# Performance work log

Hardware: AMD Instinct MI355X
Metric: run time of the kernel (lower is better)

Reference implementation:

```python
import jax, jax.numpy as jnp
import numpy as np

P = 8      # patch_size
DIM = 16   # per-head channel dim
HEADS = 4
LN_EPS = 1e-6


def _conv_patch(x, W, b):
    # stride=kernel=P patch conv; SAME degenerates to VALID when H%P==0
    y = jax.lax.conv_general_dilated(
        x, W, window_strides=(P, P), padding='VALID',
        dimension_numbers=('NHWC', 'HWIO', 'NHWC'))
    return y + b


def _proj_heads(x, W, b):
    # b h w (c p0 p1 head) -> b head (h p0) (w p1) c
    y = _conv_patch(x, W, b)
    B, hh, ww, _ = y.shape
    y = y.reshape(B, hh, ww, DIM, P, P, HEADS)
    y = y.transpose(0, 6, 1, 4, 2, 5, 3)            # b head hh p0 ww p1 c
    return y.reshape(B, HEADS, hh * P, ww * P, DIM)


def _to_patch(t):
    # n head (h p1) (w p2) c -> n head c h w p1 p2
    B, hd, H, W, c = t.shape
    t = t.reshape(B, hd, H // P, P, W // P, P, c)
    return t.transpose(0, 1, 6, 2, 4, 3, 5)


def _from_patch(t):
    # n head c h w p1 p2 -> n head (h p1) (w p2) c
    B, hd, c, hh, ww, _, _ = t.shape
    t = t.transpose(0, 1, 3, 5, 4, 6, 2)
    return t.reshape(B, hd, hh * P, ww * P, c)


def setup_inputs() -> dict:
    key = jax.random.key(0)
    ks = jax.random.split(key, 6)
    B, H, W, Cin = 4, 256, 256, 16
    feat = DIM * HEADS * P * P  # 4096
    s_qkv = 0.02
    inp = {
        'x': jax.random.normal(ks[0], (B, H, W, Cin), jnp.float32),
        'Wq': jax.random.normal(ks[1], (P, P, Cin, feat), jnp.float32) * s_qkv,
        'bq': jnp.zeros((feat,), jnp.float32),
        'Wk': jax.random.normal(ks[2], (P, P, Cin, feat), jnp.float32) * s_qkv,
        'bk': jnp.zeros((feat,), jnp.float32),
        'Wv': jax.random.normal(ks[3], (P, P, Cin, feat), jnp.float32) * s_qkv,
        'bv': jnp.zeros((feat,), jnp.float32),
        'ln_scale': jnp.ones((DIM,), jnp.float32),
        'ln_bias': jnp.zeros((DIM,), jnp.float32),
        'Wout': jax.random.normal(ks[4], (P, P, HEADS * DIM, DIM * P * P), jnp.float32) * 0.02,
        'bout': jnp.zeros((DIM * P * P,), jnp.float32),
    }
    return inp


def reference(x, Wq, bq, Wk, bk, Wv, bv, ln_scale, ln_bias, Wout, bout):
    q = _proj_heads(x, Wq, bq)  # [B, heads, H, W, dim]
    k = _proj_heads(x, Wk, bk)
    v = _proj_heads(x, Wv, bv)

    # frequency-domain 'attention': per-8x8-patch rfft2 multiply irfft2
    qf = jnp.fft.rfft2(_to_patch(q))
    kf = jnp.fft.rfft2(_to_patch(k))
    out = jnp.fft.irfft2(qf * kf, s=(P, P))
    out = _from_patch(out)                          # [B, heads, H, W, dim]

    # LayerNorm over channel dim (flax default eps=1e-6, scale+bias)
    mu = out.mean(-1, keepdims=True)
    var = ((out - mu) ** 2).mean(-1, keepdims=True)
    out = (out - mu) * jax.lax.rsqrt(var + LN_EPS) * ln_scale + ln_bias

    out = v * out
    # b head h w c -> b h w (head c)
    B, hd, H, W, c = out.shape
    out = out.transpose(0, 2, 3, 1, 4).reshape(B, H, W, hd * c)

    # output projection (no heads): conv then b h w (c p0 p1) -> b (h p0) (w p1) c
    y = _conv_patch(out, Wout, bout)
    Bo, hh, ww, _ = y.shape
    y = y.reshape(Bo, hh, ww, DIM, P, P).transpose(0, 1, 4, 2, 5, 3)
    return y.reshape(Bo, hh * P, ww * P, DIM)
```

## Files before the change

kernel.cpp:

```cpp
#include <hip/hip_runtime.h>
#include <hip/hip_bf16.h>
#include <cstdint>
#include <cstddef>

typedef float  f32x4  __attribute__((ext_vector_type(4)));
typedef __bf16 bf16x8 __attribute__((ext_vector_type(8)));
typedef __bf16 bf16x4 __attribute__((ext_vector_type(4)));


#define GLOAD_LDS16(gp, lp)                                                     \
    __builtin_amdgcn_global_load_lds(                                           \
        (const __attribute__((address_space(1))) void*)(gp),                    \
        (__attribute__((address_space(3))) void*)(lp), 16, 0, 0)

#define MFMA16(d, a, b) d = __builtin_amdgcn_mfma_f32_16x16x32_bf16(a, b, d, 0, 0, 0)

#define BAR() asm volatile("s_barrier" ::: "memory")

__global__ __launch_bounds__(256) void k_im2col(const float* __restrict__ x,
                                                __bf16* __restrict__ Xb)
{
    const int p = blockIdx.x;
    const int t = threadIdx.x;
    const int b = p >> 10, hh = (p >> 5) & 31, ww = p & 31;
    const int e = t * 4;
    const int c = e & 15, ij = e >> 4;
    const int i = ij >> 3, j = ij & 7;
    const size_t src = ((((size_t)(b * 256 + hh * 8 + i)) * 256) + (ww * 8 + j)) * 16 + c;
    f32x4 v = *(const f32x4*)(x + src);
    bf16x4 o;
    o[0] = (__bf16)v[0]; o[1] = (__bf16)v[1]; o[2] = (__bf16)v[2]; o[3] = (__bf16)v[3];
    *(bf16x4*)(Xb + (size_t)p * 1024 + e) = o;
}

__global__ __launch_bounds__(256) void k_wqkvT(const float* __restrict__ Wq,
                                               const float* __restrict__ Wk,
                                               const float* __restrict__ Wv,
                                               __bf16* __restrict__ WT)
{
    __shared__ float tile[64][261];
    int q = blockIdx.x;
    const int t = threadIdx.x;
    const int kb = q & 15;   q >>= 4;
    const int ch = q & 15;   q >>= 4;
    const int s  = q;
    const int k0 = kb * 64;
    const float* __restrict__ W = (s == 0) ? Wq : (s == 1) ? Wk : Wv;

#pragma unroll
    for (int rep = 0; rep < 16; rep++) {
        const int idx = rep * 256 + t;
        const int kl = idx >> 6, col4 = (idx & 63) * 4;
        const f32x4 v = *(const f32x4*)(W + (size_t)(k0 + kl) * 4096 + ch * 256 + col4);
        tile[kl][col4 + 0] = v[0];
        tile[kl][col4 + 1] = v[1];
        tile[kl][col4 + 2] = v[2];
        tile[kl][col4 + 3] = v[3];
    }
    __syncthreads();
    const size_t nbase = (size_t)s * 4096 + ch * 64;
#pragma unroll
    for (int rep = 0; rep < 64; rep++) {
        const int idx = rep * 256 + t;
        const int kl = idx & 63;
        const int rest = idx >> 6;
        const int p = rest & 63, h = rest >> 6;
        WT[(nbase + h * 1024 + p) * 1024 + k0 + kl] = (__bf16)tile[kl][p * 4 + h];
    }
}

__global__ __launch_bounds__(256) void k_biasperm(const float* __restrict__ bq,
                                                  const float* __restrict__ bk,
                                                  const float* __restrict__ bv,
                                                  float* __restrict__ bp)
{
    const int n = blockIdx.x * 256 + threadIdx.x;
    const int s = n >> 12;
    const int r = n & 4095;
    const int head = r >> 10, c = (r >> 6) & 15, pp = r & 63;
    const float* __restrict__ b = (s == 0) ? bq : (s == 1) ? bk : bv;
    bp[n] = b[c * 256 + pp * 4 + head];
}

__global__ __launch_bounds__(256) void k_woutT(const float* __restrict__ Wo,
                                               __bf16* __restrict__ WT)
{
    __shared__ float tile[64][129];
    const int q = blockIdx.x;
    const int t = threadIdx.x;
    const int n0 = (q & 15) * 64;
    const int k0 = (q >> 4) * 128;
    const int ch = n0 >> 6;
#pragma unroll
    for (int rep = 0; rep < 32; rep++) {
        const int idx = rep * 256 + t;
        const int kl = idx >> 6, nn = idx & 63;
        tile[nn][kl] = Wo[(size_t)(k0 + kl) * 1024 + n0 + nn];
    }
    __syncthreads();
#pragma unroll
    for (int rep = 0; rep < 32; rep++) {
        const int idx = rep * 256 + t;
        const int nn = idx >> 7, kl = idx & 127;
        const int no = ((nn >> 3) & 7) * 128 + (nn & 7) * 16 + ch;
        WT[(size_t)no * 4096 + k0 + kl] = (__bf16)tile[nn][kl];
    }
}

__device__ __forceinline__ void stage_half(const __bf16* __restrict__ mat,
                                           const int gRow0, const int K,
                                           const int k0, __bf16* lds, const int t)
{
    const int w6 = (t >> 6) << 6;
#pragma unroll
    for (int r = 0; r < 2; r++) {
        const int idx = r * 512 + t;
        const int row = idx >> 3;
        const int colb = ((t & 7) << 4) ^ ((row & 7) << 4);
        const char* gp = (const char*)(mat + (size_t)(gRow0 + row) * K + k0) + colb;
        GLOAD_LDS16(gp, (char*)lds + (size_t)(r * 512 + w6) * 16);
    }
}

__global__ __launch_bounds__(512, 1) void gemm256(const __bf16* __restrict__ A,
                                                  const __bf16* __restrict__ Bt,
                                                  __bf16* __restrict__ C,
                                                  const float* __restrict__ bias,
                                                  const int M, const int N,
                                                  const int K, const int nby)
{
    __shared__ __bf16 As[2][256 * 64];
    __shared__ __bf16 Bs[2][256 * 64];

    const int t = threadIdx.x;
    const int l = t & 63, w = t >> 6;
    const int wr = w >> 2, wc = w & 3;

    const int nwg = (int)gridDim.x, cpx = nwg >> 3;
    const int bid = (int)blockIdx.x;
    const int sbid = (bid & 7) * cpx + (bid >> 3);
    const int bm = sbid % nby, bn = sbid / nby;
    const int row0 = bm * 256, col0 = bn * 256;

    const int lrow = l & 15;
    const int lkb  = (l >> 4) << 4;
    const int lswz = (l & 7) << 4;
    const int ce0 = ((0  + lkb) ^ lswz) >> 1;
    const int ce1 = ((64 + lkb) ^ lswz) >> 1;

    const int arow = wr * 128 + lrow;
    const int brow = wc * 64 + lrow;

    const int NT = K >> 6;
    f32x4 acc[8][4] = {};
    bf16x8 a0[4][2], a1[4][2], b[4][2];

    stage_half(A,  row0,       K, 0,  As[0],        t);
    stage_half(A,  row0 + 128, K, 0,  As[0] + 8192, t);
    stage_half(A,  row0,       K, 64, As[1],        t);
    stage_half(A,  row0 + 128, K, 64, As[1] + 8192, t);
    stage_half(Bt, col0,       K, 0,  Bs[0],        t);
    stage_half(Bt, col0 + 128, K, 0,  Bs[0] + 8192, t);
    asm volatile("s_waitcnt vmcnt(0)" ::: "memory");
    BAR();
#pragma unroll
    for (int mi = 0; mi < 4; ++mi) {
        const int rr = (arow + mi * 16) * 64;
        a0[mi][0] = *(const bf16x8*)&As[0][rr + ce0];
        a0[mi][1] = *(const bf16x8*)&As[0][rr + ce1];
    }

    int cur = 0;
    for (int it = 0; it < NT; ++it) {
        const __bf16* AsC = As[cur];
        const __bf16* AsN = As[cur ^ 1];
        const __bf16* BsC = Bs[cur];
        __bf16* BsN = Bs[cur ^ 1];
        const bool stB = (it + 1 < NT);
        const bool stA = (it + 2 < NT);
        const bool pfA = (it + 1 < NT);
        const int kB = (it + 1) << 6;
        const int kA = (it + 2) << 6;

        BAR();
#pragma unroll
        for (int ni = 0; ni < 4; ++ni) {
            const int rr = (brow + ni * 16) * 64;
            b[ni][0] = *(const bf16x8*)&BsC[rr + ce0];
            b[ni][1] = *(const bf16x8*)&BsC[rr + ce1];
        }
#pragma unroll
        for (int mi = 0; mi < 4; ++mi) {
            const int rr = (arow + 64 + mi * 16) * 64;
            a1[mi][0] = *(const bf16x8*)&AsC[rr + ce0];
            a1[mi][1] = *(const bf16x8*)&AsC[rr + ce1];
        }
        if (stB) {
            stage_half(Bt, col0,       K, kB, BsN,        t);
            stage_half(Bt, col0 + 128, K, kB, BsN + 8192, t);
        }
        __builtin_amdgcn_s_setprio(1);
#pragma unroll
        for (int mi = 0; mi < 4; ++mi)
#pragma unroll
            for (int ni = 0; ni < 4; ++ni) {
                MFMA16(acc[mi][ni], a0[mi][0], b[ni][0]);
                MFMA16(acc[mi][ni], a0[mi][1], b[ni][1]);
            }
        __builtin_amdgcn_s_setprio(0);
        if (pfA)
            asm volatile("s_waitcnt vmcnt(4)" ::: "memory");

        BAR();
        if (pfA) {
#pragma unroll
            for (int mi = 0; mi < 4; ++mi) {
                const int rr = (arow + mi * 16) * 64;
                a0[mi][0] = *(const bf16x8*)&AsN[rr + ce0];
                a0[mi][1] = *(const bf16x8*)&AsN[rr + ce1];
            }
        }
        if (stA) {
            stage_half(A, row0,       K, kA, As[cur],        t);
            stage_half(A, row0 + 128, K, kA, As[cur] + 8192, t);
        }
        __builtin_amdgcn_s_setprio(1);
#pragma unroll
        for (int mi = 0; mi < 4; ++mi)
#pragma unroll
            for (int ni = 0; ni < 4; ++ni) {
                MFMA16(acc[4 + mi][ni], a1[mi][0], b[ni][0]);
                MFMA16(acc[4 + mi][ni], a1[mi][1], b[ni][1]);
            }
        __builtin_amdgcn_s_setprio(0);
        if (stB) {
            if (stA) asm volatile("s_waitcnt vmcnt(4)" ::: "memory");
            else     asm volatile("s_waitcnt vmcnt(0)" ::: "memory");
        }

        cur ^= 1;
    }

    const int rbase = row0 + wr * 128;
    const int cbase = col0 + wc * 64;
    const int jr = (l >> 4) * 4;
#pragma unroll
    for (int m = 0; m < 8; ++m)
#pragma unroll
        for (int n = 0; n < 4; ++n) {
            const int cw = cbase + n * 16 + lrow;
            const float bsv = bias[cw];
#pragma unroll
            for (int j = 0; j < 4; ++j) {
                const int rw = rbase + m * 16 + jr + j;
                C[(size_t)rw * N + cw] = (__bf16)(acc[m][n][j] + bsv);
            }
        }
}

template <int BN>
__global__ __launch_bounds__(256, 3) void gemm_splitk(const __bf16* __restrict__ A,
                                                      const __bf16* __restrict__ Bt,
                                                      float* __restrict__ Pout,
                                                      const int K, const int kc)
{
    constexpr int BM  = 128, BK = 64;
    constexpr int NF  = BN / 32;
    constexpr int APW = (BM * BK / 512) / 4;
    constexpr int BPW = (BN * BK / 512) / 4;
    __shared__ __bf16 As[BM * BK];
    __shared__ __bf16 Bs[BN * BK];

    const int t = threadIdx.x;
    const int l = t & 63, w = t >> 6;

    const int nwg  = (int)gridDim.x;
    const int cpx  = nwg >> 3;
    const int bid  = (int)blockIdx.x;
    const int sbid = (bid & 7) * cpx + (bid >> 3);
    const int bm = sbid >> 4;
    const int ks = (sbid >> 3) & 1;
    const int bn = sbid & 7;
    const int row0 = bm * BM, col0 = bn * BN;
    const int kstart = ks * kc;

    const int wr = w >> 1, wc = w & 1;
    const int lr = l & 15;
    const int lk = (l >> 4) * 8;
    const int srow = l >> 3;
    const int scol = (l & 7) * 8;

    f32x4 acc[4][NF] = {};

    for (int k0 = kstart; k0 < kstart + kc; k0 += BK) {
        __syncthreads();
#pragma unroll
        for (int p = 0; p < APW; p++) {
            const int chunk = w * APW + p;
            const __bf16* gp = A + (size_t)(row0 + chunk * 8 + srow) * K + k0 + scol;
            GLOAD_LDS16(gp, &As[chunk * 512]);
        }
#pragma unroll
        for (int p = 0; p < BPW; p++) {
            const int chunk = w * BPW + p;
            const __bf16* gp = Bt + (size_t)(col0 + chunk * 8 + srow) * K + k0 + scol;
            GLOAD_LDS16(gp, &Bs[chunk * 512]);
        }
        __syncthreads();
#pragma unroll
        for (int kk = 0; kk < 2; kk++) {
            bf16x8 af[4], bfr[NF];
#pragma unroll
            for (int m = 0; m < 4; m++)
                af[m] = *(const bf16x8*)&As[(wr * 64 + m * 16 + lr) * BK + kk * 32 + lk];
#pragma unroll
            for (int n = 0; n < NF; n++)
                bfr[n] = *(const bf16x8*)&Bs[(wc * (BN / 2) + n * 16 + lr) * BK + kk * 32 + lk];
#pragma unroll
            for (int m = 0; m < 4; m++)
#pragma unroll
                for (int n = 0; n < NF; n++)
                    acc[m][n] = __builtin_amdgcn_mfma_f32_16x16x32_bf16(
                        af[m], bfr[n], acc[m][n], 0, 0, 0);
        }
    }

    float* __restrict__ P = Pout + (size_t)ks * 4194304;
    const int rbase = row0 + wr * 64;
    const int cbase = col0 + wc * (BN / 2);
#pragma unroll
    for (int m = 0; m < 4; m++)
#pragma unroll
        for (int n = 0; n < NF; n++) {
            const int cw = cbase + n * 16 + lr;
#pragma unroll
            for (int j = 0; j < 4; j++) {
                const int rw = rbase + m * 16 + (l >> 4) * 4 + j;
                P[(size_t)rw * 1024 + cw] = acc[m][n][j];
            }
        }
}

__global__ __launch_bounds__(256) void k_redscatter(const float* __restrict__ P,
                                                    const float* __restrict__ bo,
                                                    float* __restrict__ Y)
{
    const int i = (blockIdx.x * 256 + threadIdx.x) * 4;
    const int rw = i >> 10, cw = i & 1023;
    const f32x4 v0 = *(const f32x4*)(P + i);
    const f32x4 v1 = *(const f32x4*)(P + 4194304 + i);
    const int p0 = cw >> 7, low = cw & 127;
    const int b = rw >> 10, hh = (rw >> 5) & 31, wwp = rw & 31;
    float* dst = Y + (size_t)(b * 256 + hh * 8 + p0) * 4096 + wwp * 128 + low;
    f32x4 o;
#pragma unroll
    for (int j = 0; j < 4; j++) {
        const int c = cw + j;
        o[j] = v0[j] + v1[j] + bo[((c & 15) << 6) + ((c >> 7) << 3) + ((c >> 4) & 7)];
    }
    *(f32x4*)dst = o;
}

__global__ __launch_bounds__(128) void k_freqconv(const __bf16* __restrict__ C1,
                                                  const float* __restrict__ lns,
                                                  const float* __restrict__ lnb,
                                                  __bf16* __restrict__ Z)
{
    const int blk = blockIdx.x;
    const int p = blk >> 2, head = blk & 3;
    const int t = threadIdx.x;

    __shared__ float qs[16 * 68];
    __shared__ float ks[16 * 68];
    __shared__ float vs[16 * 68];
    __shared__ float os[16 * 68];

    const __bf16* __restrict__ base = C1 + (size_t)p * 12288 + head * 1024;
    {
        const int cl = t >> 3, off = (t & 7) * 8;
        const bf16x8 vq = *(const bf16x8*)(base + cl * 64 + off);
        const bf16x8 vk = *(const bf16x8*)(base + 4096 + cl * 64 + off);
        const bf16x8 vv = *(const bf16x8*)(base + 8192 + cl * 64 + off);
#pragma unroll
        for (int e = 0; e < 8; e++) {
            qs[cl * 68 + off + e] = (float)vq[e];
            ks[cl * 68 + off + e] = (float)vk[e];
            vs[cl * 68 + off + e] = (float)vv[e];
        }
    }
    __syncthreads();

    const int cc = t >> 3, p0 = t & 7;
    float outr[8] = {0.f, 0.f, 0.f, 0.f, 0.f, 0.f, 0.f, 0.f};
#pragma unroll
    for (int i0 = 0; i0 < 8; i0++) {
        const int kr = (p0 - i0) & 7;
        const f32x4 qa = *(const f32x4*)&qs[cc * 68 + i0 * 8];
        const f32x4 qb = *(const f32x4*)&qs[cc * 68 + i0 * 8 + 4];
        const f32x4 ka = *(const f32x4*)&ks[cc * 68 + kr * 8];
        const f32x4 kb = *(const f32x4*)&ks[cc * 68 + kr * 8 + 4];
        const float qrow[8] = {qa[0], qa[1], qa[2], qa[3], qb[0], qb[1], qb[2], qb[3]};
        const float krow[8] = {ka[0], ka[1], ka[2], ka[3], kb[0], kb[1], kb[2], kb[3]};
#pragma unroll
        for (int j = 0; j < 8; j++) {
            const float qv = qrow[j];
#pragma unroll
            for (int p1 = 0; p1 < 8; p1++)
                outr[p1] = fmaf(qv, krow[(p1 - j) & 7], outr[p1]);
        }
    }
#pragma unroll
    for (int e = 0; e < 8; e++)
        os[cc * 68 + p0 * 8 + e] = outr[e];
    __syncthreads();

    if (t < 64) {
        const int pp = t;
        float o[16];
        float mu = 0.f;
#pragma unroll
        for (int c2 = 0; c2 < 16; c2++) { o[c2] = os[c2 * 68 + pp]; mu += o[c2]; }
        mu *= 0.0625f;
        float var = 0.f;
#pragma unroll
        for (int c2 = 0; c2 < 16; c2++) { const float d = o[c2] - mu; var = fmaf(d, d, var); }
        var *= 0.0625f;
        const float rs = rsqrtf(var + 1e-6f);
        bf16x8 z0, z1;
#pragma unroll
        for (int c2 = 0; c2 < 16; c2++) {
            float zv = (o[c2] - mu) * rs * lns[c2] + lnb[c2];
            zv *= vs[c2 * 68 + pp];
            if (c2 < 8) z0[c2] = (__bf16)zv; else z1[c2 - 8] = (__bf16)zv;
        }
        bf16x8* zp = (bf16x8*)(Z + (size_t)p * 4096 + pp * 64 + head * 16);
        zp[0] = z0;
        zp[1] = z1;
    }
}

extern "C" void kernel_launch(void* const* d_in, const int* in_sizes, int n_in,
                              void* d_out, int out_size, void* d_ws, size_t ws_size,
                              hipStream_t stream)
{
    const float* x   = (const float*)d_in[0];
    const float* Wq  = (const float*)d_in[1];
    const float* bq  = (const float*)d_in[2];
    const float* Wk  = (const float*)d_in[3];
    const float* bk  = (const float*)d_in[4];
    const float* Wv  = (const float*)d_in[5];
    const float* bv  = (const float*)d_in[6];
    const float* lns = (const float*)d_in[7];
    const float* lnb = (const float*)d_in[8];
    const float* Wo  = (const float*)d_in[9];
    const float* bo  = (const float*)d_in[10];
    float* out = (float*)d_out;

    char* ws = (char*)d_ws;
    __bf16* Xb    = (__bf16*)(ws);
    __bf16* WqkvT = (__bf16*)(ws + 8388608);
    float*  bperm = (float*) (ws + 33554432);
    __bf16* WoutT = (__bf16*)(ws + 33603584);
    __bf16* C1    = (__bf16*)(ws + 41992192);
    __bf16* Z     = (__bf16*)(ws + 142655488);
    float*  Ppart = (float*) (ws + 41992192);

    k_im2col  <<<dim3(4096), dim3(256), 0, stream>>>(x, Xb);
    k_wqkvT   <<<dim3(768),  dim3(256), 0, stream>>>(Wq, Wk, Wv, WqkvT);
    k_biasperm<<<dim3(48),   dim3(256), 0, stream>>>(bq, bk, bv, bperm);
    k_woutT   <<<dim3(512),  dim3(256), 0, stream>>>(Wo, WoutT);

    gemm256<<<dim3(768), dim3(512), 0, stream>>>(Xb, WqkvT, C1, bperm,
                                                 4096, 12288, 1024, 16);

    k_freqconv<<<dim3(16384), dim3(128), 0, stream>>>(C1, lns, lnb, Z);

    gemm_splitk<128><<<dim3(512), dim3(256), 0, stream>>>(Z, WoutT, Ppart,
                                                          4096, 2048);

    k_redscatter<<<dim3(4096), dim3(256), 0, stream>>>(Ppart, bo, out);
}
```

Before: 231.7 us.

## Merge prep kernels into one launch and raise output GEMM split-K to four

The four preprocessing kernels (im2col, QKV weight transpose, bias permute, output-weight transpose) become one kernel that dispatches on block index, which saves three launches. The output-projection GEMM moves from split-K 2 to split-K 4 with twice the workgroups and occupancy hint 4, so more of the GPU is busy. The reduction kernel now sums four partial buffers, adding partial-buffer traffic. The merged prep kernel reserves the largest shared-memory tile for every block, which may reduce occupancy for the light im2col blocks.

```diff
diff --git a/kernel.cpp b/kernel.cpp
--- a/kernel.cpp
+++ b/kernel.cpp
@@ -17,93 +17,87 @@
 
 #define BAR() asm volatile("s_barrier" ::: "memory")
 
-__global__ __launch_bounds__(256) void k_im2col(const float* __restrict__ x,
-                                                __bf16* __restrict__ Xb)
-{
-    const int p = blockIdx.x;
+__global__ __launch_bounds__(256) void k_prep(const float* __restrict__ x,
+                                              const float* __restrict__ Wq,
+                                              const float* __restrict__ Wk,
+                                              const float* __restrict__ Wv,
+                                              const float* __restrict__ bq,
+                                              const float* __restrict__ bk,
+                                              const float* __restrict__ bv,
+                                              const float* __restrict__ Wo,
+                                              __bf16* __restrict__ Xb,
+                                              __bf16* __restrict__ WT,
+                                              float* __restrict__ bp,
+                                              __bf16* __restrict__ WoT)
+{
+    __shared__ float smem[64 * 261];
+    const int blk = (int)blockIdx.x;
     const int t = threadIdx.x;
-    const int b = p >> 10, hh = (p >> 5) & 31, ww = p & 31;
-    const int e = t * 4;
-    const int c = e & 15, ij = e >> 4;
-    const int i = ij >> 3, j = ij & 7;
-    const size_t src = ((((size_t)(b * 256 + hh * 8 + i)) * 256) + (ww * 8 + j)) * 16 + c;
-    f32x4 v = *(const f32x4*)(x + src);
-    bf16x4 o;
-    o[0] = (__bf16)v[0]; o[1] = (__bf16)v[1]; o[2] = (__bf16)v[2]; o[3] = (__bf16)v[3];
-    *(bf16x4*)(Xb + (size_t)p * 1024 + e) = o;
-}
-
-__global__ __launch_bounds__(256) void k_wqkvT(const float* __restrict__ Wq,
-                                               const float* __restrict__ Wk,
-                                               const float* __restrict__ Wv,
-                                               __bf16* __restrict__ WT)
-{
-    __shared__ float tile[64][261];
-    int q = blockIdx.x;
-    const int t = threadIdx.x;
-    const int kb = q & 15;   q >>= 4;
-    const int ch = q & 15;   q >>= 4;
-    const int s  = q;
-    const int k0 = kb * 64;
-    const float* __restrict__ W = (s == 0) ? Wq : (s == 1) ? Wk : Wv;
-
-#pragma unroll
-    for (int rep = 0; rep < 16; rep++) {
-        const int idx = rep * 256 + t;
-        const int kl = idx >> 6, col4 = (idx & 63) * 4;
-        const f32x4 v = *(const f32x4*)(W + (size_t)(k0 + kl) * 4096 + ch * 256 + col4);
-        tile[kl][col4 + 0] = v[0];
-        tile[kl][col4 + 1] = v[1];
-        tile[kl][col4 + 2] = v[2];
-        tile[kl][col4 + 3] = v[3];
-    }
-    __syncthreads();
-    const size_t nbase = (size_t)s * 4096 + ch * 64;
-#pragma unroll
-    for (int rep = 0; rep < 64; rep++) {
-        const int idx = rep * 256 + t;
-        const int kl = idx & 63;
-        const int rest = idx >> 6;
-        const int p = rest & 63, h = rest >> 6;
-        WT[(nbase + h * 1024 + p) * 1024 + k0 + kl] = (__bf16)tile[kl][p * 4 + h];
-    }
-}
-
-__global__ __launch_bounds__(256) void k_biasperm(const float* __restrict__ bq,
-                                                  const float* __restrict__ bk,
-                                                  const float* __restrict__ bv,
-                                                  float* __restrict__ bp)
-{
-    const int n = blockIdx.x * 256 + threadIdx.x;
-    const int s = n >> 12;
-    const int r = n & 4095;
-    const int head = r >> 10, c = (r >> 6) & 15, pp = r & 63;
-    const float* __restrict__ b = (s == 0) ? bq : (s == 1) ? bk : bv;
-    bp[n] = b[c * 256 + pp * 4 + head];
-}
-
-__global__ __launch_bounds__(256) void k_woutT(const float* __restrict__ Wo,
-                                               __bf16* __restrict__ WT)
-{
-    __shared__ float tile[64][129];
-    const int q = blockIdx.x;
-    const int t = threadIdx.x;
-    const int n0 = (q & 15) * 64;
-    const int k0 = (q >> 4) * 128;
-    const int ch = n0 >> 6;
-#pragma unroll
-    for (int rep = 0; rep < 32; rep++) {
-        const int idx = rep * 256 + t;
-        const int kl = idx >> 6, nn = idx & 63;
-        tile[nn][kl] = Wo[(size_t)(k0 + kl) * 1024 + n0 + nn];
-    }
-    __syncthreads();
-#pragma unroll
-    for (int rep = 0; rep < 32; rep++) {
-        const int idx = rep * 256 + t;
-        const int nn = idx >> 7, kl = idx & 127;
-        const int no = ((nn >> 3) & 7) * 128 + (nn & 7) * 16 + ch;
-        WT[(size_t)no * 4096 + k0 + kl] = (__bf16)tile[nn][kl];
+
+    if (blk < 4096) {
+        const int p = blk;
+        const int b = p >> 10, hh = (p >> 5) & 31, ww = p & 31;
+        const int e = t * 4;
+        const int c = e & 15, ij = e >> 4;
+        const int i = ij >> 3, j = ij & 7;
+        const size_t src = ((((size_t)(b * 256 + hh * 8 + i)) * 256) + (ww * 8 + j)) * 16 + c;
+        f32x4 v = *(const f32x4*)(x + src);
+        bf16x4 o;
+        o[0] = (__bf16)v[0]; o[1] = (__bf16)v[1]; o[2] = (__bf16)v[2]; o[3] = (__bf16)v[3];
+        *(bf16x4*)(Xb + (size_t)p * 1024 + e) = o;
+    } else if (blk < 4864) {
+        int q = blk - 4096;
+        const int kb = q & 15;   q >>= 4;
+        const int ch = q & 15;   q >>= 4;
+        const int s  = q;
+        const int k0 = kb * 64;
+        const float* __restrict__ W = (s == 0) ? Wq : (s == 1) ? Wk : Wv;
+#pragma unroll
+        for (int rep = 0; rep < 16; rep++) {
+            const int idx = rep * 256 + t;
+            const int kl = idx >> 6, col4 = (idx & 63) * 4;
+            const f32x4 v = *(const f32x4*)(W + (size_t)(k0 + kl) * 4096 + ch * 256 + col4);
+            smem[kl * 261 + col4 + 0] = v[0];
+            smem[kl * 261 + col4 + 1] = v[1];
+            smem[kl * 261 + col4 + 2] = v[2];
+            smem[kl * 261 + col4 + 3] = v[3];
+        }
+        __syncthreads();
+        const size_t nbase = (size_t)s * 4096 + ch * 64;
+#pragma unroll
+        for (int rep = 0; rep < 64; rep++) {
+            const int idx = rep * 256 + t;
+            const int kl = idx & 63;
+            const int rest = idx >> 6;
+            const int p = rest & 63, h = rest >> 6;
+            WT[(nbase + h * 1024 + p) * 1024 + k0 + kl] = (__bf16)smem[kl * 261 + p * 4 + h];
+        }
+    } else if (blk < 4912) {
+        const int n = (blk - 4864) * 256 + t;
+        const int s = n >> 12;
+        const int r = n & 4095;
+        const int head = r >> 10, c = (r >> 6) & 15, pp = r & 63;
+        const float* __restrict__ b = (s == 0) ? bq : (s == 1) ? bk : bv;
+        bp[n] = b[c * 256 + pp * 4 + head];
+    } else {
+        const int q = blk - 4912;
+        const int n0 = (q & 15) * 64;
+        const int k0 = (q >> 4) * 128;
+        const int ch = n0 >> 6;
+#pragma unroll
+        for (int rep = 0; rep < 32; rep++) {
+            const int idx = rep * 256 + t;
+            const int kl = idx >> 6, nn = idx & 63;
+            smem[nn * 129 + kl] = Wo[(size_t)(k0 + kl) * 1024 + n0 + nn];
+        }
+        __syncthreads();
+#pragma unroll
+        for (int rep = 0; rep < 32; rep++) {
+            const int idx = rep * 256 + t;
+            const int nn = idx >> 7, kl = idx & 127;
+            const int no = ((nn >> 3) & 7) * 128 + (nn & 7) * 16 + ch;
+            WoT[(size_t)no * 4096 + k0 + kl] = (__bf16)smem[nn * 129 + kl];
+        }
     }
 }
 
@@ -259,7 +253,7 @@
 }
 
 template <int BN>
-__global__ __launch_bounds__(256, 3) void gemm_splitk(const __bf16* __restrict__ A,
+__global__ __launch_bounds__(256, 4) void gemm_splitk(const __bf16* __restrict__ A,
                                                       const __bf16* __restrict__ Bt,
                                                       float* __restrict__ Pout,
                                                       const int K, const int kc)
@@ -278,8 +272,8 @@
     const int cpx  = nwg >> 3;
     const int bid  = (int)blockIdx.x;
     const int sbid = (bid & 7) * cpx + (bid >> 3);
-    const int bm = sbid >> 4;
-    const int ks = (sbid >> 3) & 1;
+    const int bm = sbid >> 5;
+    const int ks = (sbid >> 3) & 3;
     const int bn = sbid & 7;
     const int row0 = bm * BM, col0 = bn * BN;
     const int kstart = ks * kc;
@@ -349,6 +343,8 @@
     const int rw = i >> 10, cw = i & 1023;
     const f32x4 v0 = *(const f32x4*)(P + i);
     const f32x4 v1 = *(const f32x4*)(P + 4194304 + i);
+    const f32x4 v2 = *(const f32x4*)(P + 8388608 + i);
+    const f32x4 v3 = *(const f32x4*)(P + 12582912 + i);
     const int p0 = cw >> 7, low = cw & 127;
     const int b = rw >> 10, hh = (rw >> 5) & 31, wwp = rw & 31;
     float* dst = Y + (size_t)(b * 256 + hh * 8 + p0) * 4096 + wwp * 128 + low;
@@ -356,7 +352,8 @@
 #pragma unroll
     for (int j = 0; j < 4; j++) {
         const int c = cw + j;
-        o[j] = v0[j] + v1[j] + bo[((c & 15) << 6) + ((c >> 7) << 3) + ((c >> 4) & 7)];
+        o[j] = (v0[j] + v1[j]) + (v2[j] + v3[j])
+             + bo[((c & 15) << 6) + ((c >> 7) << 3) + ((c >> 4) & 7)];
     }
     *(f32x4*)dst = o;
 }
@@ -465,18 +462,16 @@
     __bf16* Z     = (__bf16*)(ws + 142655488);
     float*  Ppart = (float*) (ws + 41992192);
 
-    k_im2col  <<<dim3(4096), dim3(256), 0, stream>>>(x, Xb);
-    k_wqkvT   <<<dim3(768),  dim3(256), 0, stream>>>(Wq, Wk, Wv, WqkvT);
-    k_biasperm<<<dim3(48),   dim3(256), 0, stream>>>(bq, bk, bv, bperm);
-    k_woutT   <<<dim3(512),  dim3(256), 0, stream>>>(Wo, WoutT);
+    k_prep<<<dim3(5424), dim3(256), 0, stream>>>(x, Wq, Wk, Wv, bq, bk, bv, Wo,
+                                                 Xb, WqkvT, bperm, WoutT);
 
     gemm256<<<dim3(768), dim3(512), 0, stream>>>(Xb, WqkvT, C1, bperm,
                                                  4096, 12288, 1024, 16);
 
     k_freqconv<<<dim3(16384), dim3(128), 0, stream>>>(C1, lns, lnb, Z);
 
-    gemm_splitk<128><<<dim3(512), dim3(256), 0, stream>>>(Z, WoutT, Ppart,
-                                                          4096, 2048);
+    gemm_splitk<128><<<dim3(1024), dim3(256), 0, stream>>>(Z, WoutT, Ppart,
+                                                           4096, 1024);
 
     k_redscatter<<<dim3(4096), dim3(256), 0, stream>>>(Ppart, bo, out);
 }
```

Result: no change. 227.2 us (median of 2 runs) (-1.9%).
